# Optimization experiments

Hardware: AMD Instinct MI355X
Metric: run time of the kernel (lower is better)

## Reference

```python
import jax, jax.numpy as jnp
import numpy as np

T, B, OBS, LS, H, NA = 256, 1024, 128, 128, 128, 18


def setup_inputs() -> dict:
    key = jax.random.key(0)
    ks = jax.random.split(key, 20)
    rn = lambda i, shape, sc: jax.random.normal(ks[i], shape, dtype=jnp.float32) * sc
    return {
        "x": jax.random.normal(ks[0], (T * B, OBS), dtype=jnp.float32),
        "done": (jax.random.uniform(ks[1], (T * B,)) < 0.05).astype(jnp.float32),
        "h0": rn(2, (1, B, H), 0.1),
        "c0": rn(3, (1, B, H), 0.1),
        # MLP encoder: obs -> 128 -> 32 -> lstm_size
        "W1": rn(4, (128, OBS), 0.1), "b1": jnp.zeros((128,), jnp.float32),
        "W2": rn(5, (32, 128), 0.1), "b2": jnp.zeros((32,), jnp.float32),
        "W3": rn(6, (LS, 32), 0.1), "b3": jnp.zeros((LS,), jnp.float32),
        # LSTM params, PyTorch gate order [i, f, g, o]
        "Wih": rn(7, (4 * H, LS), 0.1), "Whh": rn(8, (4 * H, H), 0.1),
        "bih": jnp.zeros((4 * H,), jnp.float32), "bhh": jnp.zeros((4 * H,), jnp.float32),
        "Wa": rn(9, (NA, H), 0.01), "ba": jnp.zeros((NA,), jnp.float32),
        "Wc": rn(10, (1, H), 0.1), "bc": jnp.zeros((1,), jnp.float32),
    }


def reference(x, done, h0, c0, W1, b1, W2, b2, W3, b3, Wih, Whh, bih, bhh, Wa, ba, Wc, bc):
    # MLP encoder (self.network)
    hid = jax.nn.relu(x @ W1.T + b1)
    hid = jax.nn.relu(hid @ W2.T + b2)
    hid = jax.nn.relu(hid @ W3.T + b3)           # [T*B, LS]
    Bsz = h0.shape[1]
    hid = hid.reshape(-1, Bsz, hid.shape[-1])    # [T, B, LS]
    d = done.reshape(-1, Bsz)                    # [T, B]

    Hh = h0.shape[-1]

    def step(carry, inp):
        h, c = carry
        xt, dt = inp
        m = (1.0 - dt)[:, None]                  # reset mask
        h = h * m
        c = c * m
        gates = xt @ Wih.T + bih + h @ Whh.T + bhh   # [B, 4H]
        i = jax.nn.sigmoid(gates[:, :Hh])
        f = jax.nn.sigmoid(gates[:, Hh:2 * Hh])
        g = jnp.tanh(gates[:, 2 * Hh:3 * Hh])
        o = jax.nn.sigmoid(gates[:, 3 * Hh:])
        c = f * c + i * g
        h = o * jnp.tanh(c)
        return (h, c), h

    (hN, cN), hs = jax.lax.scan(step, (h0[0], c0[0]), (hid, d))
    flat = hs.reshape(-1, Hh)                    # [T*B, H]
    logits = flat @ Wa.T + ba                    # actor head
    value = flat @ Wc.T + bc                     # critic head
    return jnp.concatenate([logits, value], axis=-1)  # [T*B, NA+1]
```

## Files before the change

### kernel.cpp

```cpp
#include <hip/hip_runtime.h>
#include <hip/hip_bf16.h>

typedef unsigned short u16;
typedef unsigned int u32;
typedef __attribute__((ext_vector_type(8))) short short8;
typedef __attribute__((ext_vector_type(4))) float f4;
typedef __attribute__((ext_vector_type(4))) u32 u4;
typedef __attribute__((ext_vector_type(2))) u32 u2;

#define MFMA(a, b, c) __builtin_amdgcn_mfma_f32_16x16x32_bf16((a), (b), (c), 0, 0, 0)

#define TT 256
#define BB 1024
#define NN (TT * BB)
#define SC1 1.4426950408889634f
#define SC2 2.8853900817779268f

#define OFF_W1  0
#define OFF_W2  16384
#define OFF_W3  20480
#define OFF_WIH 24576
#define OFF_WHH 90112
#define OFF_WA  155648
#define WF_TOT  159744

#define WS_HS_OFF 134217728
#define WS_WF_OFF 167772160
#define WS_NEED_BIG 335863808ULL

static __device__ __forceinline__ u16 f2bf(float f) {
    u32 u = __float_as_uint(f);
    u32 r = (u + 0x7FFFu + ((u >> 16) & 1u)) >> 16;
    return (u16)r;
}
static __device__ __forceinline__ short8 pack8(f4 a, f4 b) {
    short8 r;
    r[0] = (short)f2bf(a[0]); r[1] = (short)f2bf(a[1]);
    r[2] = (short)f2bf(a[2]); r[3] = (short)f2bf(a[3]);
    r[4] = (short)f2bf(b[0]); r[5] = (short)f2bf(b[1]);
    r[6] = (short)f2bf(b[2]); r[7] = (short)f2bf(b[3]);
    return r;
}
static __device__ __forceinline__ short8 u4_to_s8(u4 v) {
    union { u4 u; short8 s; } t; t.u = v; return t.s;
}
static __device__ __forceinline__ float sig2(float x) {
    return __builtin_amdgcn_rcpf(1.f + __builtin_amdgcn_exp2f(-x));
}
static __device__ __forceinline__ float tanh2pre(float x) {
    return 2.f * __builtin_amdgcn_rcpf(1.f + __builtin_amdgcn_exp2f(-x)) - 1.f;
}
static __device__ __forceinline__ float tanh_c(float x) {
    return 2.f * __builtin_amdgcn_rcpf(1.f + __builtin_amdgcn_exp2f(-SC2 * x)) - 1.f;
}
static __device__ __forceinline__ void lds_barrier() {
    asm volatile("s_waitcnt lgkmcnt(0)\n\ts_barrier" ::: "memory");
}

static __device__ void convW128(const float* src, int Nn, u16* dst, int tid, int nth) {
    int tot = Nn * 128;
    for (int d = tid; d < tot; d += nth) {
        int j = d & 7, l = (d >> 3) & 63, ck = d >> 9;
        int kc = ck & 3, nt = ck >> 2;
        int n = nt * 16 + (l & 15), k = kc * 32 + ((l >> 4) << 3) + j;
        dst[d] = f2bf(src[n * 128 + k]);
    }
}
static __device__ void convW128s(const float* src, u16* dst, int tid, int nth) {
    int tot = 512 * 128;
    for (int d = tid; d < tot; d += nth) {
        int j = d & 7, l = (d >> 3) & 63, ck = d >> 9;
        int kc = ck & 3, nt = ck >> 2;
        int n = nt * 16 + (l & 15), k = kc * 32 + ((l >> 4) << 3) + j;
        float s = ((n >> 7) == 2) ? SC2 : SC1;
        dst[d] = f2bf(src[n * 128 + k] * s);
    }
}
static __device__ void convW32(const float* src, int Nn, u16* dst, int tid, int nth) {
    int tot = Nn * 32;
    for (int d = tid; d < tot; d += nth) {
        int j = d & 7, l = (d >> 3) & 63, nt = d >> 9;
        int n = nt * 16 + (l & 15), k = ((l >> 4) << 3) + j;
        dst[d] = f2bf(src[n * 32 + k]);
    }
}

__global__ void k0_conv(const float* __restrict__ W1, const float* __restrict__ W2,
                        const float* __restrict__ W3, const float* __restrict__ Wih,
                        const float* __restrict__ Whh, const float* __restrict__ Wa,
                        const float* __restrict__ Wc, u16* __restrict__ wf) {
    int tid = blockIdx.x * blockDim.x + threadIdx.x;
    int nth = gridDim.x * blockDim.x;
    convW128(W1, 128, wf + OFF_W1, tid, nth);
    convW128(W2, 32, wf + OFF_W2, tid, nth);
    convW32(W3, 128, wf + OFF_W3, tid, nth);
    convW128s(Wih, wf + OFF_WIH, tid, nth);
    convW128s(Whh, wf + OFF_WHH, tid, nth);
    for (int d = tid; d < 32 * 128; d += nth) {
        int j = d & 7, l = (d >> 3) & 63, ck = d >> 9;
        int kc = ck & 3, nt = ck >> 2;
        int n = nt * 16 + (l & 15), k = kc * 32 + ((l >> 4) << 3) + j;
        float v = (n < 18) ? Wa[n * 128 + k] : ((n == 18) ? Wc[k] : 0.f);
        wf[OFF_WA + d] = f2bf(v);
    }
}

__global__ __launch_bounds__(256) void k1_fused(
    const float* __restrict__ x, const float* __restrict__ b1, const float* __restrict__ b2,
    const float* __restrict__ b3, const float* __restrict__ bih, const float* __restrict__ bhh,
    const u16* __restrict__ wf, u2* __restrict__ xg) {
    __shared__ __align__(16) u16 scr[4][2560];
    __shared__ float biasL[512];

    int tid = threadIdx.x, wv = tid >> 6, lane = tid & 63;
    int m = lane & 15, q = lane >> 4;
    u16* s1 = scr[wv];
    u16* s2 = scr[wv] + 2048;
    const short8* W1v = (const short8*)(wf + OFF_W1);
    const short8* W2v = (const short8*)(wf + OFF_W2);
    const short8* W3v = (const short8*)(wf + OFF_W3);
    const short8* WIv = (const short8*)(wf + OFF_WIH);
    int c = blockIdx.x * 4 + wv;

    for (int i = tid; i < 512; i += 256)
        biasL[i] = (bih[i] + bhh[i]) * (((i >> 7) == 2) ? SC2 : SC1);

    short8 a1[4];
    const float* xr = x + (size_t)(c * 16 + m) * 128 + q * 8;
#pragma unroll
    for (int kc = 0; kc < 4; ++kc) {
        f4 f0 = *(const f4*)(xr + kc * 32);
        f4 f1 = *(const f4*)(xr + kc * 32 + 4);
        a1[kc] = pack8(f0, f1);
    }
#pragma unroll
    for (int nt = 0; nt < 8; ++nt) {
        f4 acc = {0.f, 0.f, 0.f, 0.f};
#pragma unroll
        for (int kc = 0; kc < 4; ++kc) acc = MFMA(a1[kc], W1v[(nt * 4 + kc) * 64 + lane], acc);
        int col = nt * 16 + m;
        float bb = b1[col];
        int base = (col >> 5) * 512 + ((col >> 3) & 3) * 128 + (col & 7);
#pragma unroll
        for (int p = 0; p < 4; ++p) {
            float v = acc[p] + bb; v = v > 0.f ? v : 0.f;
            s1[base + (q * 4 + p) * 8] = f2bf(v);
        }
    }
    short8 a2[4];
#pragma unroll
    for (int kc = 0; kc < 4; ++kc) a2[kc] = *(const short8*)(s1 + kc * 512 + lane * 8);
#pragma unroll
    for (int nt = 0; nt < 2; ++nt) {
        f4 acc = {0.f, 0.f, 0.f, 0.f};
#pragma unroll
        for (int kc = 0; kc < 4; ++kc) acc = MFMA(a2[kc], W2v[(nt * 4 + kc) * 64 + lane], acc);
        int col = nt * 16 + m;
        float bb = b2[col];
        int base = (col >> 3) * 128 + (col & 7);
#pragma unroll
        for (int p = 0; p < 4; ++p) {
            float v = acc[p] + bb; v = v > 0.f ? v : 0.f;
            s2[base + (q * 4 + p) * 8] = f2bf(v);
        }
    }
    short8 a3 = *(const short8*)(s2 + lane * 8);
#pragma unroll
    for (int nt = 0; nt < 8; ++nt) {
        f4 acc = {0.f, 0.f, 0.f, 0.f};
        acc = MFMA(a3, W3v[nt * 64 + lane], acc);
        int col = nt * 16 + m;
        float bb = b3[col];
        int base = (col >> 5) * 512 + ((col >> 3) & 3) * 128 + (col & 7);
#pragma unroll
        for (int p = 0; p < 4; ++p) {
            float v = acc[p] + bb; v = v > 0.f ? v : 0.f;
            s1[base + (q * 4 + p) * 8] = f2bf(v);
        }
    }
    __syncthreads();

    short8 bfr[4];
#pragma unroll
    for (int kc = 0; kc < 4; ++kc) bfr[kc] = *(const short8*)(s1 + kc * 512 + lane * 8);
    size_t R = (size_t)c * 16 + m;
#pragma unroll
    for (int uw = 0; uw < 8; ++uw) {
        f4 acc[4];
#pragma unroll
        for (int g = 0; g < 4; ++g) acc[g] = (f4){0.f, 0.f, 0.f, 0.f};
#pragma unroll
        for (int kc = 0; kc < 4; ++kc) {
#pragma unroll
            for (int g = 0; g < 4; ++g) {
                int nt = g * 8 + uw;
                acc[g] = MFMA(WIv[(nt * 4 + kc) * 64 + lane], bfr[kc], acc[g]);
            }
        }
        u4 st0, st1;
#pragma unroll
        for (int p = 0; p < 4; ++p) {
            int u = uw * 16 + 4 * q + p;
            u32 lo = ((u32)f2bf(acc[1][p] + biasL[128 + u]) << 16) |
                     (u32)f2bf(acc[0][p] + biasL[u]);
            u32 hi = ((u32)f2bf(acc[3][p] + biasL[384 + u]) << 16) |
                     (u32)f2bf(acc[2][p] + biasL[256 + u]);
            if (p < 2) { st0[2 * p] = lo; st0[2 * p + 1] = hi; }
            else       { st1[2 * (p - 2)] = lo; st1[2 * (p - 2) + 1] = hi; }
        }
        u4* dst = (u4*)(xg + R * 128 + uw * 16 + 4 * q);
        dst[0] = st0;
        dst[1] = st1;
    }
}

__global__ __launch_bounds__(512) void k3_scan(
    const u2* __restrict__ xg, u16* __restrict__ hs, const u16* __restrict__ wf,
    const float* __restrict__ done, const float* __restrict__ h0, const float* __restrict__ c0) {
    __shared__ __align__(16) u16 hbuf[2][16 * 136];
    __shared__ __align__(16) float pre[4 * 516];
    __shared__ float dls[1024];

    int tid = threadIdx.x, wv = tid >> 6, lane = tid & 63;
    int m = lane & 15, q = lane >> 4;
    int rb = blockIdx.x * 4;
    const short8* WHv = (const short8*)(wf + OFF_WHH);

    short8 wh[4][4];
#pragma unroll
    for (int g = 0; g < 4; ++g)
#pragma unroll
        for (int kc = 0; kc < 4; ++kc)
            wh[g][kc] = WHv[(((g * 8 + wv) * 4) + kc) * 64 + lane];

    for (int i = tid; i < 2 * 12 * 136; i += 512) {
        int b = i / 1632, rem = i % 1632;
        hbuf[b][(4 + rem / 136) * 136 + (rem % 136)] = 0;
    }
    for (int i = tid; i < 1024; i += 512)
        dls[i] = 1.0f - done[(size_t)(i >> 2) * BB + rb + (i & 3)];

    int r = tid >> 7, u = tid & 127;
    float cst = c0[(size_t)(rb + r) * 128 + u];
    hbuf[0][r * 136 + u] = f2bf(h0[(size_t)(rb + r) * 128 + u]);

    u2 xp0 = xg[(size_t)blockIdx.x * 512 + tid];
    u2 xp1 = xg[(size_t)131072 + (size_t)blockIdx.x * 512 + tid];
    __syncthreads();

    for (int t = 0; t < TT; ++t) {
        const u16* hc = hbuf[t & 1];
        u16* hn = hbuf[(t + 1) & 1];
        short8 bh[4];
#pragma unroll
        for (int kc = 0; kc < 4; ++kc)
            bh[kc] = *(const short8*)(hc + m * 136 + kc * 32 + q * 8);
        f4 aH[4];
#pragma unroll
        for (int g = 0; g < 4; ++g) aH[g] = (f4){0.f, 0.f, 0.f, 0.f};
#pragma unroll
        for (int kc = 0; kc < 4; ++kc)
#pragma unroll
            for (int g = 0; g < 4; ++g) aH[g] = MFMA(wh[g][kc], bh[kc], aH[g]);

        int tp = (t + 2 < TT) ? (t + 2) : (TT - 1);
        u2 xnew = xg[(size_t)tp * 131072 + (size_t)blockIdx.x * 512 + tid];

        if (m < 4) {
#pragma unroll
            for (int g = 0; g < 4; ++g)
#pragma unroll
                for (int p = 0; p < 4; ++p)
                    pre[m * 516 + (wv * 16 + 4 * q + p) * 4 + g] = aH[g][p];
        }
        lds_barrier();

        f4 pv = *(const f4*)(pre + r * 516 + u * 4);
        float mm = dls[t * 4 + r];
        u32 w0 = xp0[0], w1 = xp0[1];
        float ip = __uint_as_float(w0 << 16)          + mm * pv[0];
        float fp = __uint_as_float(w0 & 0xFFFF0000u)  + mm * pv[1];
        float gp = __uint_as_float(w1 << 16)          + mm * pv[2];
        float op = __uint_as_float(w1 & 0xFFFF0000u)  + mm * pv[3];
        float ii = sig2(ip), ff = sig2(fp), gg = tanh2pre(gp), oo = sig2(op);
        float cc = ff * (mm * cst) + ii * gg;
        cst = cc;
        float hh = oo * tanh_c(cc);
        u16 hb = f2bf(hh);
        hn[r * 136 + u] = hb;
        hs[((size_t)t * BB + rb + r) * 128 + u] = hb;
        xp0 = xp1; xp1 = xnew;
        lds_barrier();
    }
}

__global__ __launch_bounds__(256) void k4_heads_plain(
    const u16* __restrict__ hs, const u16* __restrict__ wf,
    const float* __restrict__ ba, const float* __restrict__ bc, float* __restrict__ out) {
    int tid = threadIdx.x, wv = tid >> 6, lane = tid & 63;
    int m = lane & 15, q = lane >> 4;
    int wid = blockIdx.x * 4 + wv;
    const short8* WAv = (const short8*)(wf + OFF_WA);
    short8 wab[2][4];
#pragma unroll
    for (int nt = 0; nt < 2; ++nt)
#pragma unroll
        for (int kc = 0; kc < 4; ++kc) wab[nt][kc] = WAv[(nt * 4 + kc) * 64 + lane];
    for (int it = 0; it < 8; ++it) {
        int c = wid + it * 2048;
        const u16* row = hs + ((size_t)c * 16 + m) * 128 + q * 8;
        short8 a[4];
#pragma unroll
        for (int kc = 0; kc < 4; ++kc) a[kc] = *(const short8*)(row + kc * 32);
#pragma unroll
        for (int nt = 0; nt < 2; ++nt) {
            f4 acc = {0.f, 0.f, 0.f, 0.f};
#pragma unroll
            for (int kc = 0; kc < 4; ++kc) acc = MFMA(a[kc], wab[nt][kc], acc);
            int col = nt * 16 + m;
            if (col < 19) {
                float bb = (col < 18) ? ba[col] : bc[0];
#pragma unroll
                for (int p = 0; p < 4; ++p)
                    out[(size_t)(c * 16 + q * 4 + p) * 19 + col] = acc[p] + bb;
            }
        }
    }
}

__global__ __launch_bounds__(256) void k1_enc(
    const float* __restrict__ x, const float* __restrict__ b1, const float* __restrict__ b2,
    const float* __restrict__ b3, const u16* __restrict__ wf, u16* __restrict__ hid3f) {
    __shared__ __align__(16) u16 scr[4][2560];
    int tid = threadIdx.x, wv = tid >> 6, lane = tid & 63;
    int m = lane & 15, q = lane >> 4;
    u16* s1 = scr[wv];
    u16* s2 = scr[wv] + 2048;
    const short8* W1v = (const short8*)(wf + OFF_W1);
    const short8* W2v = (const short8*)(wf + OFF_W2);
    const short8* W3v = (const short8*)(wf + OFF_W3);
    int c = blockIdx.x * 4 + wv;
    short8 a1[4];
    const float* xr = x + (size_t)(c * 16 + m) * 128 + q * 8;
#pragma unroll
    for (int kc = 0; kc < 4; ++kc) {
        f4 f0 = *(const f4*)(xr + kc * 32);
        f4 f1 = *(const f4*)(xr + kc * 32 + 4);
        a1[kc] = pack8(f0, f1);
    }
#pragma unroll
    for (int nt = 0; nt < 8; ++nt) {
        f4 acc = {0.f, 0.f, 0.f, 0.f};
#pragma unroll
        for (int kc = 0; kc < 4; ++kc) acc = MFMA(a1[kc], W1v[(nt * 4 + kc) * 64 + lane], acc);
        int col = nt * 16 + m;
        float bb = b1[col];
        int base = (col >> 5) * 512 + ((col >> 3) & 3) * 128 + (col & 7);
#pragma unroll
        for (int p = 0; p < 4; ++p) {
            float v = acc[p] + bb; v = v > 0.f ? v : 0.f;
            s1[base + (q * 4 + p) * 8] = f2bf(v);
        }
    }
    short8 a2[4];
#pragma unroll
    for (int kc = 0; kc < 4; ++kc) a2[kc] = *(const short8*)(s1 + kc * 512 + lane * 8);
#pragma unroll
    for (int nt = 0; nt < 2; ++nt) {
        f4 acc = {0.f, 0.f, 0.f, 0.f};
#pragma unroll
        for (int kc = 0; kc < 4; ++kc) acc = MFMA(a2[kc], W2v[(nt * 4 + kc) * 64 + lane], acc);
        int col = nt * 16 + m;
        float bb = b2[col];
        int base = (col >> 3) * 128 + (col & 7);
#pragma unroll
        for (int p = 0; p < 4; ++p) {
            float v = acc[p] + bb; v = v > 0.f ? v : 0.f;
            s2[base + (q * 4 + p) * 8] = f2bf(v);
        }
    }
    short8 a3 = *(const short8*)(s2 + lane * 8);
#pragma unroll
    for (int nt = 0; nt < 8; ++nt) {
        f4 acc = {0.f, 0.f, 0.f, 0.f};
        acc = MFMA(a3, W3v[nt * 64 + lane], acc);
        int col = nt * 16 + m;
        float bb = b3[col];
        int base = (col >> 5) * 512 + ((col >> 3) & 3) * 128 + (col & 7);
#pragma unroll
        for (int p = 0; p < 4; ++p) {
            float v = acc[p] + bb; v = v > 0.f ? v : 0.f;
            s1[base + (q * 4 + p) * 8] = f2bf(v);
        }
    }
    u4* dst = (u4*)hid3f + (size_t)c * 256;
#pragma unroll
    for (int kc = 0; kc < 4; ++kc) dst[kc * 64 + lane] = *(const u4*)(s1 + kc * 512 + lane * 8);
}

__global__ __launch_bounds__(512) void k3_lstm(
    u16* __restrict__ hws, const u16* __restrict__ wf, const float* __restrict__ bih,
    const float* __restrict__ bhh, const float* __restrict__ done,
    const float* __restrict__ h0, const float* __restrict__ c0) {
    __shared__ __align__(16) u16 hbuf[2][2048];
    __shared__ __align__(16) float dls[4096];
    int tid = threadIdx.x, wv = tid >> 6, lane = tid & 63;
    int u15 = lane & 15, q = lane >> 4;
    int u = wv * 16 + u15;
    int rb = blockIdx.x * 16;
    const short8* WHv = (const short8*)(wf + OFF_WHH);
    const short8* WIv = (const short8*)(wf + OFF_WIH);
    short8 wh[4][4], wi[4][4];
#pragma unroll
    for (int g = 0; g < 4; ++g)
#pragma unroll
        for (int kc = 0; kc < 4; ++kc) {
            int nt = g * 8 + wv;
            wh[g][kc] = WHv[(nt * 4 + kc) * 64 + lane];
            wi[g][kc] = WIv[(nt * 4 + kc) * 64 + lane];
        }
    float bg[4];
#pragma unroll
    for (int g = 0; g < 4; ++g)
        bg[g] = (bih[g * 128 + u] + bhh[g * 128 + u]) * ((g == 2) ? SC2 : SC1);
    for (int i = tid; i < 4096; i += 512) {
        int t = i >> 4, r = i & 15;
        dls[i] = 1.0f - done[(size_t)t * BB + rb + r];
    }
    float cst[4];
#pragma unroll
    for (int k = 0; k < 4; ++k) {
        int r = 4 * q + k;
        cst[k] = c0[(size_t)(rb + r) * 128 + u];
        float hv = h0[(size_t)(rb + r) * 128 + u];
        hbuf[0][(u >> 5) * 512 + (((u >> 3) & 3) * 16 + r) * 8 + (u & 7)] = f2bf(hv);
    }
    const u4* h3 = (const u4*)hws;
    u4 xf[4];
#pragma unroll
    for (int kc = 0; kc < 4; ++kc) xf[kc] = h3[((size_t)blockIdx.x * 4 + kc) * 64 + lane];
    __syncthreads();
    for (int t = 0; t < TT; ++t) {
        const u16* hc = hbuf[t & 1];
        u16* hn = hbuf[(t + 1) & 1];
        short8 ah[4];
#pragma unroll
        for (int kc = 0; kc < 4; ++kc) ah[kc] = *(const short8*)(hc + kc * 512 + lane * 8);
        f4 aH[4], aX[4];
#pragma unroll
        for (int g = 0; g < 4; ++g) { aH[g] = (f4){0.f, 0.f, 0.f, 0.f}; aX[g] = (f4){0.f, 0.f, 0.f, 0.f}; }
#pragma unroll
        for (int kc = 0; kc < 4; ++kc) {
            short8 xs = u4_to_s8(xf[kc]);
#pragma unroll
            for (int g = 0; g < 4; ++g) {
                aH[g] = MFMA(ah[kc], wh[g][kc], aH[g]);
                aX[g] = MFMA(xs, wi[g][kc], aX[g]);
            }
        }
        if (t < TT - 1) {
#pragma unroll
            for (int kc = 0; kc < 4; ++kc)
                xf[kc] = h3[(((size_t)(t + 1) * 64 + blockIdx.x) * 4 + kc) * 64 + lane];
        }
        f4 dm = *(const f4*)(dls + t * 16 + 4 * q);
#pragma unroll
        for (int k = 0; k < 4; ++k) {
            float mm = dm[k];
            float ip = aX[0][k] + bg[0] + mm * aH[0][k];
            float fp = aX[1][k] + bg[1] + mm * aH[1][k];
            float gp = aX[2][k] + bg[2] + mm * aH[2][k];
            float op = aX[3][k] + bg[3] + mm * aH[3][k];
            float ii = sig2(ip), ff = sig2(fp), gg = tanh2pre(gp), oo = sig2(op);
            float cc = ff * (mm * cst[k]) + ii * gg;
            cst[k] = cc;
            float hh = oo * tanh_c(cc);
            hn[(u >> 5) * 512 + (((u >> 3) & 3) * 16 + (4 * q + k)) * 8 + (u & 7)] = f2bf(hh);
        }
        lds_barrier();
        if (wv < 4) {
            u4 v = *(const u4*)(hn + wv * 512 + lane * 8);
            ((u4*)hws)[(((size_t)t * 64 + blockIdx.x) * 4 + wv) * 64 + lane] = v;
        }
    }
}

__global__ __launch_bounds__(256) void k4_heads_frag(
    const u16* __restrict__ hsf, const u16* __restrict__ wf,
    const float* __restrict__ ba, const float* __restrict__ bc, float* __restrict__ out) {
    int tid = threadIdx.x, wv = tid >> 6, lane = tid & 63;
    int m = lane & 15, q = lane >> 4;
    int wid = blockIdx.x * 4 + wv;
    const short8* WAv = (const short8*)(wf + OFF_WA);
    short8 wab[2][4];
#pragma unroll
    for (int nt = 0; nt < 2; ++nt)
#pragma unroll
        for (int kc = 0; kc < 4; ++kc) wab[nt][kc] = WAv[(nt * 4 + kc) * 64 + lane];
    const short8* A = (const short8*)hsf;
    for (int it = 0; it < 8; ++it) {
        int c = wid + it * 2048;
        short8 a[4];
#pragma unroll
        for (int kc = 0; kc < 4; ++kc) a[kc] = A[((size_t)c * 4 + kc) * 64 + lane];
#pragma unroll
        for (int nt = 0; nt < 2; ++nt) {
            f4 acc = {0.f, 0.f, 0.f, 0.f};
#pragma unroll
            for (int kc = 0; kc < 4; ++kc) acc = MFMA(a[kc], wab[nt][kc], acc);
            int col = nt * 16 + m;
            if (col < 19) {
                float bb = (col < 18) ? ba[col] : bc[0];
#pragma unroll
                for (int p = 0; p < 4; ++p)
                    out[(size_t)(c * 16 + q * 4 + p) * 19 + col] = acc[p] + bb;
            }
        }
    }
}

extern "C" void kernel_launch(void* const* d_in, const int* in_sizes, int n_in,
                              void* d_out, int out_size, void* d_ws, size_t ws_size,
                              hipStream_t stream) {
    const float* x    = (const float*)d_in[0];
    const float* done = (const float*)d_in[1];
    const float* h0   = (const float*)d_in[2];
    const float* c0   = (const float*)d_in[3];
    const float* W1   = (const float*)d_in[4];
    const float* b1   = (const float*)d_in[5];
    const float* W2   = (const float*)d_in[6];
    const float* b2   = (const float*)d_in[7];
    const float* W3   = (const float*)d_in[8];
    const float* b3   = (const float*)d_in[9];
    const float* Wih  = (const float*)d_in[10];
    const float* Whh  = (const float*)d_in[11];
    const float* bih  = (const float*)d_in[12];
    const float* bhh  = (const float*)d_in[13];
    const float* Wa   = (const float*)d_in[14];
    const float* ba   = (const float*)d_in[15];
    const float* Wc   = (const float*)d_in[16];
    const float* bc   = (const float*)d_in[17];
    float* out = (float*)d_out;
    u16* ws = (u16*)d_ws;

    if (ws_size >= WS_NEED_BIG) {
        u2*  xg = (u2*)ws;
        u16* hs = ws + WS_HS_OFF;
        u16* wf = ws + WS_WF_OFF;
        hipLaunchKernelGGL(k0_conv, dim3(128), dim3(256), 0, stream,
                           W1, W2, W3, Wih, Whh, Wa, Wc, wf);
        hipLaunchKernelGGL(k1_fused, dim3(4096), dim3(256), 0, stream,
                           x, b1, b2, b3, bih, bhh, wf, xg);
        hipLaunchKernelGGL(k3_scan, dim3(256), dim3(512), 0, stream,
                           xg, hs, wf, done, h0, c0);
        hipLaunchKernelGGL(k4_heads_plain, dim3(512), dim3(256), 0, stream,
                           hs, wf, ba, bc, out);
    } else {
        u16* hid3f = ws;
        u16* wf    = ws + (size_t)NN * 128;
        hipLaunchKernelGGL(k0_conv, dim3(128), dim3(256), 0, stream,
                           W1, W2, W3, Wih, Whh, Wa, Wc, wf);
        hipLaunchKernelGGL(k1_enc, dim3(4096), dim3(256), 0, stream,
                           x, b1, b2, b3, wf, hid3f);
        hipLaunchKernelGGL(k3_lstm, dim3(64), dim3(512), 0, stream,
                           hid3f, wf, bih, bhh, done, h0, c0);
        hipLaunchKernelGGL(k4_heads_frag, dim3(512), dim3(256), 0, stream,
                           hid3f, wf, ba, bc, out);
    }
}
```

Before: 598.8 us.

## Transpose input-gate GEMM output layout and restructure scan pre-activation exchange

The input projection kernel now swaps the MFMA operands, so the xg buffer is stored row-major per batch row, with one u2 of four packed gate values per unit. The scan kernel now reads xg with natural row/unit indexing instead of per-block tiling. The shared pre-activation exchange is rewritten as gate-major rows written with f4 vector stores. The time loop is unrolled by two with fixed buffer pointers, and the next-step prefetch is moved after the barrier. The goal is fewer scattered LDS stores per step and simpler addressing, at the cost of strided 8-byte global stores in the projection kernel and four scalar LDS reads per thread.

```diff
diff --git a/kernel.cpp b/kernel.cpp
--- a/kernel.cpp
+++ b/kernel.cpp
@@ -180,37 +180,31 @@
     }
     __syncthreads();
 
-    short8 bfr[4];
-#pragma unroll
-    for (int kc = 0; kc < 4; ++kc) bfr[kc] = *(const short8*)(s1 + kc * 512 + lane * 8);
-    size_t R = (size_t)c * 16 + m;
+    short8 afr[4];
+#pragma unroll
+    for (int kc = 0; kc < 4; ++kc) afr[kc] = *(const short8*)(s1 + kc * 512 + lane * 8);
 #pragma unroll
     for (int uw = 0; uw < 8; ++uw) {
         f4 acc[4];
 #pragma unroll
         for (int g = 0; g < 4; ++g) acc[g] = (f4){0.f, 0.f, 0.f, 0.f};
 #pragma unroll
-        for (int kc = 0; kc < 4; ++kc) {
-#pragma unroll
-            for (int g = 0; g < 4; ++g) {
-                int nt = g * 8 + uw;
-                acc[g] = MFMA(WIv[(nt * 4 + kc) * 64 + lane], bfr[kc], acc[g]);
-            }
-        }
-        u4 st0, st1;
-#pragma unroll
-        for (int p = 0; p < 4; ++p) {
-            int u = uw * 16 + 4 * q + p;
-            u32 lo = ((u32)f2bf(acc[1][p] + biasL[128 + u]) << 16) |
-                     (u32)f2bf(acc[0][p] + biasL[u]);
-            u32 hi = ((u32)f2bf(acc[3][p] + biasL[384 + u]) << 16) |
-                     (u32)f2bf(acc[2][p] + biasL[256 + u]);
-            if (p < 2) { st0[2 * p] = lo; st0[2 * p + 1] = hi; }
-            else       { st1[2 * (p - 2)] = lo; st1[2 * (p - 2) + 1] = hi; }
-        }
-        u4* dst = (u4*)(xg + R * 128 + uw * 16 + 4 * q);
-        dst[0] = st0;
-        dst[1] = st1;
+        for (int kc = 0; kc < 4; ++kc)
+#pragma unroll
+            for (int g = 0; g < 4; ++g)
+                acc[g] = MFMA(afr[kc], WIv[(((g * 8 + uw) * 4) + kc) * 64 + lane], acc[g]);
+        float bs0 = biasL[uw * 16 + m];
+        float bs1 = biasL[128 + uw * 16 + m];
+        float bs2 = biasL[256 + uw * 16 + m];
+        float bs3 = biasL[384 + uw * 16 + m];
+#pragma unroll
+        for (int p = 0; p < 4; ++p) {
+            size_t row = (size_t)c * 16 + 4 * q + p;
+            u2 pk;
+            pk[0] = ((u32)f2bf(acc[1][p] + bs1) << 16) | (u32)f2bf(acc[0][p] + bs0);
+            pk[1] = ((u32)f2bf(acc[3][p] + bs3) << 16) | (u32)f2bf(acc[2][p] + bs2);
+            xg[row * 128 + uw * 16 + m] = pk;
+        }
     }
 }
 
@@ -218,7 +212,7 @@
     const u2* __restrict__ xg, u16* __restrict__ hs, const u16* __restrict__ wf,
     const float* __restrict__ done, const float* __restrict__ h0, const float* __restrict__ c0) {
     __shared__ __align__(16) u16 hbuf[2][16 * 136];
-    __shared__ __align__(16) float pre[4 * 516];
+    __shared__ __align__(16) float pre2[16 * 132];
     __shared__ float dls[1024];
 
     int tid = threadIdx.x, wv = tid >> 6, lane = tid & 63;
@@ -244,13 +238,12 @@
     float cst = c0[(size_t)(rb + r) * 128 + u];
     hbuf[0][r * 136 + u] = f2bf(h0[(size_t)(rb + r) * 128 + u]);
 
-    u2 xp0 = xg[(size_t)blockIdx.x * 512 + tid];
-    u2 xp1 = xg[(size_t)131072 + (size_t)blockIdx.x * 512 + tid];
+    size_t xbase = (size_t)(rb + r) * 128 + u;
+    u2 xA = xg[xbase];
+    u2 xB = xg[xbase + (size_t)BB * 128];
     __syncthreads();
 
-    for (int t = 0; t < TT; ++t) {
-        const u16* hc = hbuf[t & 1];
-        u16* hn = hbuf[(t + 1) & 1];
+    auto step = [&](int t, const u16* hc, u16* hn, u2& X) {
         short8 bh[4];
 #pragma unroll
         for (int kc = 0; kc < 4; ++kc)
@@ -263,25 +256,26 @@
 #pragma unroll
             for (int g = 0; g < 4; ++g) aH[g] = MFMA(wh[g][kc], bh[kc], aH[g]);
 
-        int tp = (t + 2 < TT) ? (t + 2) : (TT - 1);
-        u2 xnew = xg[(size_t)tp * 131072 + (size_t)blockIdx.x * 512 + tid];
-
         if (m < 4) {
 #pragma unroll
             for (int g = 0; g < 4; ++g)
-#pragma unroll
-                for (int p = 0; p < 4; ++p)
-                    pre[m * 516 + (wv * 16 + 4 * q + p) * 4 + g] = aH[g][p];
+                *(f4*)(pre2 + (g * 4 + m) * 132 + wv * 16 + 4 * q) = aH[g];
         }
         lds_barrier();
 
-        f4 pv = *(const f4*)(pre + r * 516 + u * 4);
+        u32 w0 = X[0], w1 = X[1];
+        int tn = (t + 2 < TT) ? (t + 2) : (TT - 1);
+        X = xg[xbase + (size_t)tn * (BB * 128)];
+
         float mm = dls[t * 4 + r];
-        u32 w0 = xp0[0], w1 = xp0[1];
-        float ip = __uint_as_float(w0 << 16)          + mm * pv[0];
-        float fp = __uint_as_float(w0 & 0xFFFF0000u)  + mm * pv[1];
-        float gp = __uint_as_float(w1 << 16)          + mm * pv[2];
-        float op = __uint_as_float(w1 & 0xFFFF0000u)  + mm * pv[3];
+        float p0 = pre2[(0 * 4 + r) * 132 + u];
+        float p1 = pre2[(1 * 4 + r) * 132 + u];
+        float p2 = pre2[(2 * 4 + r) * 132 + u];
+        float p3 = pre2[(3 * 4 + r) * 132 + u];
+        float ip = __uint_as_float(w0 << 16)         + mm * p0;
+        float fp = __uint_as_float(w0 & 0xFFFF0000u) + mm * p1;
+        float gp = __uint_as_float(w1 << 16)         + mm * p2;
+        float op = __uint_as_float(w1 & 0xFFFF0000u) + mm * p3;
         float ii = sig2(ip), ff = sig2(fp), gg = tanh2pre(gp), oo = sig2(op);
         float cc = ff * (mm * cst) + ii * gg;
         cst = cc;
@@ -289,8 +283,12 @@
         u16 hb = f2bf(hh);
         hn[r * 136 + u] = hb;
         hs[((size_t)t * BB + rb + r) * 128 + u] = hb;
-        xp0 = xp1; xp1 = xnew;
         lds_barrier();
+    };
+
+    for (int t = 0; t < TT; t += 2) {
+        step(t,     hbuf[0], hbuf[1], xA);
+        step(t + 1, hbuf[1], hbuf[0], xB);
     }
 }
 
```

Result: no change. 592.3 us (-1.1%).
